# Performance work log

Measured on AMD Instinct MI355X. Metric: run time of the kernel, lower is better.

The kernel has to match this reference:

```python
import jax, jax.numpy as jnp
import numpy as np

B, S, C, H, W = 8, 32, 3, 256, 256


def setup_inputs() -> dict:
    key = jax.random.key(0)
    k1, k2 = jax.random.split(key)
    return {
        "input": jax.random.normal(k1, (B, S, C, H, W), dtype=jnp.float32),
        "target": jax.random.normal(k2, (B, C, H, W), dtype=jnp.float32),
    }


def _l2norm(x, axis):
    # F.normalize: x / max(||x||_2, eps)
    return x / jnp.maximum(jnp.linalg.norm(x, axis=axis, keepdims=True), 1e-12)


def _forward(input, target):
    b, s, c, h, w = input.shape
    # target: [B,C,H,W] -> permute(0,1,3,2) -> [B,C,W,H] -> flatten(1,2) -> [B, C*W, H]
    target_f = _l2norm(jnp.transpose(target, (0, 1, 3, 2)).reshape(b, c * w, h), axis=1)
    # input: [B,S,C,H,W] -> permute(0,1,2,4,3) -> [B,S,C,W,H] -> flatten(2,3) -> [B,S,C*W,H]
    input_f = _l2norm(jnp.transpose(input, (0, 1, 2, 4, 3)).reshape(b, s, c * w, h), axis=2)

    def corr_one(xf, wf):
        # xf: [S, C*W, H] as conv batch, wf: [C*W, H] as single-output-channel kernel
        y = jax.lax.conv_general_dilated(
            xf, wf[None], window_strides=(1,), padding=[(h - 1, h - 1)],
            dimension_numbers=("NCH", "OIH", "NCH"))
        return y[:, 0, :h]  # first H shift positions (overlap sizes 1..H)

    corr = jax.vmap(corr_one)(input_f, target_f)  # [B, S, H]
    corr = corr / jnp.arange(1, h + 1, dtype=input.dtype)  # mean over overlap size

    overlap = jnp.argmax(corr, axis=-1)            # [B, S] best overlap per sample
    shift = (h - 1) - overlap                      # rows to shift up by

    # out[b,s,:,r,:] = input[b,s,:,r+shift,:] for r < overlap, else 0
    h_idx = jnp.arange(h)[None, None, :] + shift[:, :, None]  # [B, S, H]
    valid = h_idx < h
    idx = jnp.clip(h_idx, 0, h - 1)[:, :, None, :, None]      # [B,S,1,H,1]
    gathered = jnp.take_along_axis(input, idx, axis=3)
    return jnp.where(valid[:, :, None, :, None], gathered, jnp.zeros((), input.dtype))


def reference(input, target):
    return _forward(input, target)
```

## Files before the change

kernel.cpp:

```cpp
#include <hip/hip_runtime.h>

#define B_ 8
#define S_ 32
#define C_ 3
#define H_ 256
#define W_ 256
#define HW_ (H_*W_)
#define CHW_ (C_*H_*W_)
#define NT_ 24
#define TILE_ELEMS 8192

typedef __attribute__((ext_vector_type(8))) short bf16x8;
typedef __attribute__((ext_vector_type(4))) float f32x4;

__device__ __forceinline__ void split2(float x, float y, unsigned &hp, unsigned &lp) {
  unsigned ux = __float_as_uint(x), uy = __float_as_uint(y);
  unsigned hx = ux & 0xFFFF0000u, hy = uy & 0xFFFF0000u;
  float lx = x - __uint_as_float(hx);
  float ly = y - __uint_as_float(hy);
  hp = (ux >> 16) | hy;
  lp = (__float_as_uint(lx) >> 16) | (__float_as_uint(ly) & 0xFFFF0000u);
}

__global__ void ct_zero(float* __restrict__ corrG) {
  int i = blockIdx.x * 256 + threadIdx.x;
  *(float4*)(corrG + i * 4) = make_float4(0.f, 0.f, 0.f, 0.f);
}

__global__ void ct_ntg(const float* __restrict__ target, float* __restrict__ rntg) {
  int r = (int)((blockIdx.x * (size_t)blockDim.x + threadIdx.x) >> 6);
  int lane = threadIdx.x & 63;
  const float* base = target + (size_t)(r >> 8) * CHW_ + (size_t)(r & 255) * W_;
  float ss = 0.f;
#pragma unroll
  for (int c = 0; c < C_; ++c)
#pragma unroll
    for (int tt = 0; tt < W_/64; ++tt) {
      float v = base[c*HW_ + tt*64 + lane];
      ss = fmaf(v, v, ss);
    }
#pragma unroll
  for (int off = 32; off; off >>= 1) ss += __shfl_xor(ss, off);
  if (lane == 0) rntg[r] = 1.0f / fmaxf(sqrtf(ss), 1e-12f);
}

__global__ void ct_bsplit(const float* __restrict__ target,
                          ushort* __restrict__ BhG, ushort* __restrict__ BlG) {
  int bx = blockIdx.x;
  int b  = bx / 24, kt = bx % 24;
  int c  = kt >> 3, w0 = (kt & 7) * 32;
  int t  = threadIdx.x;
  int trow = t >> 3, tw = t & 7;
  const float* base = target + (size_t)(b*C_ + c) * HW_ + w0 + tw*4;
  ushort* oh = BhG + (size_t)bx * TILE_ELEMS;
  ushort* ol = BlG + (size_t)bx * TILE_ELEMS;
#pragma unroll
  for (int i = 0; i < 8; ++i) {
    int row = trow + 32*i;
    float4 v = *(const float4*)(base + (size_t)row * W_);
    unsigned h0, l0, h1, l1;
    split2(v.x, v.y, h0, l0); split2(v.z, v.w, h1, l1);
    int idx = (row>>4)*512 + (tw>>1)*128 + (row&15)*8 + (tw&1)*4;
    *(uint2*)&oh[idx] = make_uint2(h0, h1);
    *(uint2*)&ol[idx] = make_uint2(l0, l1);
  }
}

__global__ __launch_bounds__(512, 4)
void ct_corr_mfma(const float* __restrict__ input,
                  const ushort* __restrict__ BhG, const ushort* __restrict__ BlG,
                  const float* __restrict__ rntg_g,
                  float* __restrict__ corrG) {
  __shared__ ushort AhL[4096], AlL[4096];
  __shared__ ushort BhL[4096], BlL[4096];
  __shared__ float ninSq[128], rnin[128], corrS[256];

  const int bx = blockIdx.x;
  const int bs = bx / 3;
  const int part = bx - bs*3;
  const int rbase = (part == 2) ? 128 : 0;
  const int cbase = (part == 0) ? 0 : 128;
  const int bG = bs >> 5;
  const int t  = threadIdx.x;
  const int lane = t & 63;
  const int wid  = t >> 6;
  const int wm   = wid >> 1;
  const int wn   = wid & 1;

  const float* Abase = input + (size_t)bs * CHW_ + (size_t)rbase * W_;
  const int panel_off = (cbase >> 4) * 512;

  if (t < 128) ninSq[t] = 0.f;
  if (t < 256) corrS[t] = 0.f;

  f32x4 acc[2][4];
#pragma unroll
  for (int m = 0; m < 2; ++m)
#pragma unroll
    for (int n = 0; n < 4; ++n) acc[m][n] = (f32x4){0.f, 0.f, 0.f, 0.f};

  float4 pa[2];
  uint4 pbh, pbl;
  float ssA[2] = {0.f, 0.f};

#define ISSUE(KT) {                                                           \
    const float* Ab = Abase + (size_t)((KT) >> 3) * HW_ + ((KT) & 7) * 32;    \
    _Pragma("unroll")                                                         \
    for (int p = 0; p < 2; ++p) {                                             \
      int f = p*512 + t;                                                      \
      pa[p] = *(const float4*)(Ab + (size_t)(f >> 3) * W_ + (f & 7) * 4);     \
    }                                                                         \
    const ushort* gB = BhG + (size_t)(bG*NT_ + (KT)) * TILE_ELEMS + panel_off;\
    const ushort* gL = BlG + (size_t)(bG*NT_ + (KT)) * TILE_ELEMS + panel_off;\
    pbh = *(const uint4*)(gB + t*8);                                          \
    pbl = *(const uint4*)(gL + t*8); }

#define STASH() {                                                             \
    _Pragma("unroll")                                                         \
    for (int p = 0; p < 2; ++p) {                                             \
      int f = p*512 + t;                                                      \
      int row = f >> 3, kk = (f & 7) * 4;                                     \
      int idx = (row>>4)*512 + (kk>>3)*128 + (row&15)*8 + (kk&7);             \
      float4 va = pa[p];                                                      \
      ssA[p] = fmaf(va.x, va.x, fmaf(va.y, va.y,                              \
               fmaf(va.z, va.z, fmaf(va.w, va.w, ssA[p]))));                  \
      unsigned h0, l0, h1, l1;                                                \
      split2(va.x, va.y, h0, l0); split2(va.z, va.w, h1, l1);                 \
      *(uint2*)&AhL[idx] = make_uint2(h0, h1);                                \
      *(uint2*)&AlL[idx] = make_uint2(l0, l1);                                \
    }                                                                         \
    *(uint4*)&BhL[t*8] = pbh;                                                 \
    *(uint4*)&BlL[t*8] = pbl; }

  ISSUE(0);

  for (int kt = 0; kt < NT_; ++kt) {
    __syncthreads();
    STASH();
    __syncthreads();
    if (kt < NT_ - 1) ISSUE(kt + 1);

    bf16x8 bh[4], bl[4];
#pragma unroll
    for (int n = 0; n < 4; ++n) {
      int ct = wn*4 + n;
      bh[n] = *(const bf16x8*)&BhL[ct*512 + lane*8];
      bl[n] = *(const bf16x8*)&BlL[ct*512 + lane*8];
    }
    __builtin_amdgcn_s_setprio(1);
#pragma unroll
    for (int m = 0; m < 2; ++m) {
      int rt = wm*2 + m;
      bf16x8 ah = *(const bf16x8*)&AhL[rt*512 + lane*8];
      bf16x8 al = *(const bf16x8*)&AlL[rt*512 + lane*8];
#pragma unroll
      for (int n = 0; n < 4; ++n) {
        acc[m][n] = __builtin_amdgcn_mfma_f32_16x16x32_bf16(ah, bh[n], acc[m][n], 0, 0, 0);
        acc[m][n] = __builtin_amdgcn_mfma_f32_16x16x32_bf16(ah, bl[n], acc[m][n], 0, 0, 0);
        acc[m][n] = __builtin_amdgcn_mfma_f32_16x16x32_bf16(al, bh[n], acc[m][n], 0, 0, 0);
      }
    }
    __builtin_amdgcn_s_setprio(0);
  }

#pragma unroll
  for (int p = 0; p < 2; ++p) {
    int row = (p*512 + t) >> 3;
    atomicAdd(&ninSq[row], ssA[p]);
  }
  __syncthreads();
  if (t < 128) rnin[t] = 1.0f / fmaxf(sqrtf(ninSq[t]), 1e-12f);
  __syncthreads();

#pragma unroll
  for (int n = 0; n < 4; ++n) {
    int col = cbase + wn*64 + n*16 + (lane & 15);
    float rc = rntg_g[bG*256 + col];
#pragma unroll
    for (int m = 0; m < 2; ++m) {
      f32x4 a = acc[m][n];
#pragma unroll
      for (int r = 0; r < 4; ++r) {
        int lrow = wm*32 + m*16 + (lane >> 4)*4 + r;
        int q = col - (rbase + lrow);
        if (q >= 0) atomicAdd(&corrS[q], a[r] * rnin[lrow] * rc);
      }
    }
  }
  __syncthreads();

  if (t < 256) atomicAdd(&corrG[bs*256 + t], corrS[t]);
}

__global__ void ct_argmax(const float* __restrict__ corrG, int* __restrict__ shift) {
  int bs = blockIdx.x;
  int lane = threadIdx.x;
  unsigned long long key = 0;
#pragma unroll
  for (int i = 0; i < 4; ++i) {
    int q = lane + 64*i;
    float v = corrG[bs*256 + q] / (float)(256 - q);
    unsigned u = __float_as_uint(v);
    u = (u & 0x80000000u) ? ~u : (u | 0x80000000u);
    unsigned long long k = ((unsigned long long)u << 32) | (unsigned)q;
    if (k > key) key = k;
  }
#pragma unroll
  for (int off = 32; off; off >>= 1) {
    unsigned long long o = __shfl_xor(key, off);
    if (o > key) key = o;
  }
  if (lane == 0) shift[bs] = (int)(key & 0xFFFFFFFFull);
}

__global__ void ct_gather(const float* __restrict__ input,
                          const int* __restrict__ shift,
                          float* __restrict__ out) {
  size_t idx = (size_t)blockIdx.x * blockDim.x + threadIdx.x;
  int w4 = (int)(idx & 63);
  int h  = (int)((idx >> 6) & 255);
  int sc = (int)(idx >> 14);
  int bs = sc / 3;
  int hh = h + shift[bs];
  float4 v = make_float4(0.f, 0.f, 0.f, 0.f);
  if (hh < H_) v = *(const float4*)(input + ((size_t)sc << 16) + (size_t)hh * W_ + w4*4);
  *(float4*)(out + (idx << 2)) = v;
}

extern "C" void kernel_launch(void* const* d_in, const int* in_sizes, int n_in,
                              void* d_out, int out_size, void* d_ws, size_t ws_size,
                              hipStream_t stream) {
  const float* input  = (const float*)d_in[0];
  const float* target = (const float*)d_in[1];
  float* out = (float*)d_out;

  float* rntg  = (float*)d_ws;
  float* corrG = rntg + 2048;
  int*   shift = (int*)(corrG + 65536);
  ushort* BhG  = (ushort*)(shift + 256);
  ushort* BlG  = BhG + (size_t)B_ * NT_ * TILE_ELEMS;

  ct_zero      <<<64, 256, 0, stream>>>(corrG);
  ct_ntg       <<<512, 256, 0, stream>>>(target, rntg);
  ct_bsplit    <<<B_ * NT_, 256, 0, stream>>>(target, BhG, BlG);
  ct_corr_mfma <<<B_ * S_ * 3, 512, 0, stream>>>(input, BhG, BlG, rntg, corrG);
  ct_argmax    <<<B_ * S_, 64, 0, stream>>>(corrG, shift);
  ct_gather    <<<(B_*S_*C_*H_*W_/4) / 256, 256, 0, stream>>>(input, shift, out);
}
```

Baseline: 204.0 us.

## Retile correlation GEMM into 64-row blocks with direct global-to-LDS B loads

```diff
diff --git a/kernel.cpp b/kernel.cpp
--- a/kernel.cpp
+++ b/kernel.cpp
@@ -12,6 +12,9 @@
 
 typedef __attribute__((ext_vector_type(8))) short bf16x8;
 typedef __attribute__((ext_vector_type(4))) float f32x4;
+typedef unsigned int u32;
+typedef u32 __attribute__((address_space(3)))* lds_u32p;
+typedef const u32 __attribute__((address_space(1)))* glb_u32p;
 
 __device__ __forceinline__ void split2(float x, float y, unsigned &hp, unsigned &lp) {
   unsigned ux = __float_as_uint(x), uy = __float_as_uint(y);
@@ -22,9 +25,8 @@
   lp = (__float_as_uint(lx) >> 16) | (__float_as_uint(ly) & 0xFFFF0000u);
 }
 
-__global__ void ct_zero(float* __restrict__ corrG) {
-  int i = blockIdx.x * 256 + threadIdx.x;
-  *(float4*)(corrG + i * 4) = make_float4(0.f, 0.f, 0.f, 0.f);
+__device__ __forceinline__ void gl2lds16(const ushort* g, ushort* l) {
+  __builtin_amdgcn_global_load_lds((glb_u32p)g, (lds_u32p)l, 16, 0, 0);
 }
 
 __global__ void ct_ntg(const float* __restrict__ target, float* __restrict__ rntg) {
@@ -70,27 +72,24 @@
 void ct_corr_mfma(const float* __restrict__ input,
                   const ushort* __restrict__ BhG, const ushort* __restrict__ BlG,
                   const float* __restrict__ rntg_g,
-                  float* __restrict__ corrG) {
-  __shared__ ushort AhL[4096], AlL[4096];
-  __shared__ ushort BhL[4096], BlL[4096];
-  __shared__ float ninSq[128], rnin[128], corrS[256];
+                  float* __restrict__ corrP) {
+  __shared__ ushort AhL[2048], AlL[2048];
+  __shared__ ushort BhL[8192], BlL[8192];
+  __shared__ float ninSq[64], rnin[64], corrS[256];
 
   const int bx = blockIdx.x;
-  const int bs = bx / 3;
-  const int part = bx - bs*3;
-  const int rbase = (part == 2) ? 128 : 0;
-  const int cbase = (part == 0) ? 0 : 128;
+  const int bs = bx >> 2;
+  const int mb = bx & 3;
   const int bG = bs >> 5;
   const int t  = threadIdx.x;
   const int lane = t & 63;
   const int wid  = t >> 6;
-  const int wm   = wid >> 1;
-  const int wn   = wid & 1;
-
-  const float* Abase = input + (size_t)bs * CHW_ + (size_t)rbase * W_;
-  const int panel_off = (cbase >> 4) * 512;
-
-  if (t < 128) ninSq[t] = 0.f;
+  const int wm   = wid >> 2;
+  const int wn   = wid & 3;
+
+  const float* Abase = input + (size_t)bs * CHW_ + (size_t)(mb * 64) * W_;
+
+  if (t < 64) ninSq[t] = 0.f;
   if (t < 256) corrS[t] = 0.f;
 
   f32x4 acc[2][4];
@@ -99,46 +98,42 @@
 #pragma unroll
     for (int n = 0; n < 4; ++n) acc[m][n] = (f32x4){0.f, 0.f, 0.f, 0.f};
 
-  float4 pa[2];
-  uint4 pbh, pbl;
-  float ssA[2] = {0.f, 0.f};
-
-#define ISSUE(KT) {                                                           \
-    const float* Ab = Abase + (size_t)((KT) >> 3) * HW_ + ((KT) & 7) * 32;    \
-    _Pragma("unroll")                                                         \
-    for (int p = 0; p < 2; ++p) {                                             \
-      int f = p*512 + t;                                                      \
-      pa[p] = *(const float4*)(Ab + (size_t)(f >> 3) * W_ + (f & 7) * 4);     \
-    }                                                                         \
-    const ushort* gB = BhG + (size_t)(bG*NT_ + (KT)) * TILE_ELEMS + panel_off;\
-    const ushort* gL = BlG + (size_t)(bG*NT_ + (KT)) * TILE_ELEMS + panel_off;\
-    pbh = *(const uint4*)(gB + t*8);                                          \
-    pbl = *(const uint4*)(gL + t*8); }
-
-#define STASH() {                                                             \
-    _Pragma("unroll")                                                         \
-    for (int p = 0; p < 2; ++p) {                                             \
-      int f = p*512 + t;                                                      \
-      int row = f >> 3, kk = (f & 7) * 4;                                     \
-      int idx = (row>>4)*512 + (kk>>3)*128 + (row&15)*8 + (kk&7);             \
-      float4 va = pa[p];                                                      \
-      ssA[p] = fmaf(va.x, va.x, fmaf(va.y, va.y,                              \
-               fmaf(va.z, va.z, fmaf(va.w, va.w, ssA[p]))));                  \
-      unsigned h0, l0, h1, l1;                                                \
-      split2(va.x, va.y, h0, l0); split2(va.z, va.w, h1, l1);                 \
-      *(uint2*)&AhL[idx] = make_uint2(h0, h1);                                \
-      *(uint2*)&AlL[idx] = make_uint2(l0, l1);                                \
-    }                                                                         \
-    *(uint4*)&BhL[t*8] = pbh;                                                 \
-    *(uint4*)&BlL[t*8] = pbl; }
-
-  ISSUE(0);
+  const int lrow = ((t >> 7) & 3) * 16 + ((t >> 1) & 15);
+  const int kk   = ((t >> 5) & 3) * 8 + (t & 1) * 4;
+  const int aidx = ((t >> 7) & 3) * 512 + ((t >> 5) & 3) * 128
+                 + ((t >> 1) & 15) * 8 + (t & 1) * 4;
+
+  float4 pa;
+  float ssA = 0.f;
+
+  pa = *(const float4*)(Abase + (size_t)lrow * W_ + kk);
 
   for (int kt = 0; kt < NT_; ++kt) {
     __syncthreads();
-    STASH();
+    {
+      const ushort* gh = BhG + (size_t)(bG*NT_ + kt) * TILE_ELEMS + wn*2048;
+      const ushort* gl = BlG + (size_t)(bG*NT_ + kt) * TILE_ELEMS + wn*2048;
+#pragma unroll
+      for (int o = 0; o < 4; ++o)
+        gl2lds16(gh + o*512 + lane*8, &BhL[wn*2048 + o*512]);
+#pragma unroll
+      for (int o = 0; o < 4; ++o)
+        gl2lds16(gl + o*512 + lane*8, &BlL[wn*2048 + o*512]);
+    }
+    {
+      float4 va = pa;
+      ssA = fmaf(va.x, va.x, fmaf(va.y, va.y,
+            fmaf(va.z, va.z, fmaf(va.w, va.w, ssA))));
+      unsigned h0, l0, h1, l1;
+      split2(va.x, va.y, h0, l0); split2(va.z, va.w, h1, l1);
+      *(uint2*)&AhL[aidx] = make_uint2(h0, h1);
+      *(uint2*)&AlL[aidx] = make_uint2(l0, l1);
+    }
     __syncthreads();
-    if (kt < NT_ - 1) ISSUE(kt + 1);
+    if (kt < NT_ - 1) {
+      const float* Ab = Abase + (size_t)((kt+1) >> 3) * HW_ + ((kt+1) & 7) * 32;
+      pa = *(const float4*)(Ab + (size_t)lrow * W_ + kk);
+    }
 
     bf16x8 bh[4], bl[4];
 #pragma unroll
@@ -147,7 +142,6 @@
       bh[n] = *(const bf16x8*)&BhL[ct*512 + lane*8];
       bl[n] = *(const bf16x8*)&BlL[ct*512 + lane*8];
     }
-    __builtin_amdgcn_s_setprio(1);
 #pragma unroll
     for (int m = 0; m < 2; ++m) {
       int rt = wm*2 + m;
@@ -160,46 +154,42 @@
         acc[m][n] = __builtin_amdgcn_mfma_f32_16x16x32_bf16(al, bh[n], acc[m][n], 0, 0, 0);
       }
     }
-    __builtin_amdgcn_s_setprio(0);
-  }
-
-#pragma unroll
-  for (int p = 0; p < 2; ++p) {
-    int row = (p*512 + t) >> 3;
-    atomicAdd(&ninSq[row], ssA[p]);
-  }
+  }
+
+  atomicAdd(&ninSq[lrow], ssA);
   __syncthreads();
-  if (t < 128) rnin[t] = 1.0f / fmaxf(sqrtf(ninSq[t]), 1e-12f);
+  if (t < 64) rnin[t] = 1.0f / fmaxf(sqrtf(ninSq[t]), 1e-12f);
   __syncthreads();
 
 #pragma unroll
   for (int n = 0; n < 4; ++n) {
-    int col = cbase + wn*64 + n*16 + (lane & 15);
+    int col = wn*64 + n*16 + (lane & 15);
     float rc = rntg_g[bG*256 + col];
 #pragma unroll
     for (int m = 0; m < 2; ++m) {
       f32x4 a = acc[m][n];
 #pragma unroll
       for (int r = 0; r < 4; ++r) {
-        int lrow = wm*32 + m*16 + (lane >> 4)*4 + r;
-        int q = col - (rbase + lrow);
-        if (q >= 0) atomicAdd(&corrS[q], a[r] * rnin[lrow] * rc);
+        int lr = wm*32 + m*16 + (lane >> 4)*4 + r;
+        int q = col - (mb*64 + lr);
+        if (q >= 0) atomicAdd(&corrS[q], a[r] * rnin[lr] * rc);
       }
     }
   }
   __syncthreads();
 
-  if (t < 256) atomicAdd(&corrG[bs*256 + t], corrS[t]);
-}
-
-__global__ void ct_argmax(const float* __restrict__ corrG, int* __restrict__ shift) {
+  if (t < 256) corrP[bs*1024 + mb*256 + t] = corrS[t];
+}
+
+__global__ void ct_argmax(const float* __restrict__ corrP, int* __restrict__ shift) {
   int bs = blockIdx.x;
   int lane = threadIdx.x;
   unsigned long long key = 0;
 #pragma unroll
   for (int i = 0; i < 4; ++i) {
     int q = lane + 64*i;
-    float v = corrG[bs*256 + q] / (float)(256 - q);
+    const float* p = corrP + bs*1024 + q;
+    float v = (p[0] + p[256] + p[512] + p[768]) / (float)(256 - q);
     unsigned u = __float_as_uint(v);
     u = (u & 0x80000000u) ? ~u : (u | 0x80000000u);
     unsigned long long k = ((unsigned long long)u << 32) | (unsigned)q;
@@ -235,15 +225,14 @@
   float* out = (float*)d_out;
 
   float* rntg  = (float*)d_ws;
-  float* corrG = rntg + 2048;
-  int*   shift = (int*)(corrG + 65536);
-  ushort* BhG  = (ushort*)(shift + 256);
+  int*   shift = (int*)(rntg + 2048);
+  float* corrP = (float*)(shift + 256);
+  ushort* BhG  = (ushort*)(corrP + 256*1024);
   ushort* BlG  = BhG + (size_t)B_ * NT_ * TILE_ELEMS;
 
-  ct_zero      <<<64, 256, 0, stream>>>(corrG);
   ct_ntg       <<<512, 256, 0, stream>>>(target, rntg);
   ct_bsplit    <<<B_ * NT_, 256, 0, stream>>>(target, BhG, BlG);
-  ct_corr_mfma <<<B_ * S_ * 3, 512, 0, stream>>>(input, BhG, BlG, rntg, corrG);
-  ct_argmax    <<<B_ * S_, 64, 0, stream>>>(corrG, shift);
+  ct_corr_mfma <<<B_ * S_ * 4, 512, 0, stream>>>(input, BhG, BlG, rntg, corrP);
+  ct_argmax    <<<B_ * S_, 64, 0, stream>>>(corrP, shift);
   ct_gather    <<<(B_*S_*C_*H_*W_/4) / 256, 256, 0, stream>>>(input, shift, out);
 }
```

Measured after the change: 227.5 us. +11.5%, slower.
